# Kernel tuning notes

Hardware: AMD Instinct MI355X
Metric: run time of the kernel (lower is better)

Reference implementation:

```python
import jax, jax.numpy as jnp
import numpy as np

K = 7
TOWERS = 4
X_SIZE = 8
POS_SIZE = 3
NUM_GRAPHS = 128
NODES_PER_GRAPH = 512
N = NUM_GRAPHS * NODES_PER_GRAPH
EPS_STD = 1e-5  # PyG StdAggregation eps
BN_EPS = 1e-5
# degree histogram passed to PNAConv.__init__ -> avg log-degree used by scalers
_DEG_HIST = np.array([0, 0, 0, 0, 0, 100, 200, 700], dtype=np.float64)
_BINS = np.arange(_DEG_HIST.shape[0], dtype=np.float64)
AVG_DEG_LOG = float((np.log(_BINS + 1.0) * _DEG_HIST).sum() / _DEG_HIST.sum())


def knn_graph(pos, num_graphs, k):
    # batched kNN (loop=False): each node gets its k nearest neighbors within its graph
    Nn, D = pos.shape
    n = Nn // num_graphs
    p = pos.reshape(num_graphs, n, D)
    d2 = jnp.sum((p[:, :, None, :] - p[:, None, :, :]) ** 2, axis=-1)  # [B,n,n]
    d2 = d2 + jnp.eye(n, dtype=d2.dtype) * 1e10  # exclude self-loops
    _, idx = jax.lax.top_k(-d2, k)  # [B,n,k] local neighbor ids
    offs = (jnp.arange(num_graphs) * n)[:, None, None]
    return (idx + offs).reshape(Nn, k)  # global source ids per target node


def pna_conv(x, nbr, W_pre, b_pre, W_post, b_post, W_lin, b_lin):
    # PyG PNAConv, towers=4, pre_layers=1, post_layers=1, divide_input=False, edge_dim=None
    Nn, F = x.shape
    k = nbr.shape[1]
    x_j = x[nbr]                                              # gather sources [N,k,F]
    x_i = jnp.broadcast_to(x[:, None, :], (Nn, k, F))         # target features
    h = jnp.concatenate([x_i, x_j], axis=-1)                  # [N,k,2F]
    m = jnp.einsum('nke,tef->nktf', h, W_pre) + b_pre         # per-tower pre-MLP [N,k,T,F]
    mean = m.mean(axis=1)
    mn = m.min(axis=1)
    mx = m.max(axis=1)
    var = jnp.mean(m * m, axis=1) - mean * mean               # PyG VarAggregation
    std = jnp.sqrt(jax.nn.relu(var) + EPS_STD)
    agg = jnp.concatenate([mean, mn, mx, std], axis=-1)       # [N,T,4F]
    amp = jnp.log(k + 1.0) / AVG_DEG_LOG                      # deg == k for every node in a knn graph
    scaled = jnp.concatenate([agg, agg * amp, agg * (1.0 / amp)], axis=-1)  # identity/amp/atten [N,T,12F]
    out = jnp.concatenate([jnp.broadcast_to(x[:, None, :], (Nn, TOWERS, F)), scaled], axis=-1)  # [N,T,13F]
    out = jnp.einsum('ntg,tgf->ntf', out, W_post) + b_post    # per-tower post-MLP [N,T,F_out]
    out = out.reshape(Nn, -1)
    return out @ W_lin + b_lin                                # mixing Linear(out,out)


def batch_norm(x, g, b):
    # training-mode BatchNorm1d over the node dimension
    mu = x.mean(axis=0)
    var = x.var(axis=0)
    return g * (x - mu) * jax.lax.rsqrt(var + BN_EPS) + b


def forward(x, pos, W_pre1, b_pre1, W_post1, b_post1, W_lin1, b_lin1, bn1_g, bn1_b,
            W_pre2, b_pre2, W_post2, b_post2, W_lin2, b_lin2, bn2_g, bn2_b, num_graphs):
    nbr = knn_graph(pos, num_graphs, K)
    h = jax.nn.relu(batch_norm(pna_conv(x, nbr, W_pre1, b_pre1, W_post1, b_post1, W_lin1, b_lin1), bn1_g, bn1_b))
    h = jax.nn.relu(batch_norm(pna_conv(h, nbr, W_pre2, b_pre2, W_post2, b_post2, W_lin2, b_lin2), bn2_g, bn2_b))
    return h.reshape(num_graphs, -1, h.shape[-1]).mean(axis=1)  # global mean pool -> [B,128]


def _winit(key, shape):
    fan_in = shape[-2]
    return (jax.random.normal(key, shape, dtype=jnp.float32) / jnp.sqrt(jnp.float32(fan_in))).astype(jnp.float32)


def setup_inputs() -> dict:
    key = jax.random.key(0)
    ks = jax.random.split(key, 8)
    F1, F2 = X_SIZE, 64
    return {
        'x': jax.random.normal(ks[0], (N, X_SIZE), dtype=jnp.float32),
        'pos': jax.random.normal(ks[1], (N, POS_SIZE), dtype=jnp.float32),
        'W_pre1': _winit(ks[2], (TOWERS, 2 * F1, F1)),
        'b_pre1': jnp.zeros((TOWERS, F1), jnp.float32),
        'W_post1': _winit(ks[3], (TOWERS, 13 * F1, 64 // TOWERS)),
        'b_post1': jnp.zeros((TOWERS, 64 // TOWERS), jnp.float32),
        'W_lin1': _winit(ks[4], (64, 64)),
        'b_lin1': jnp.zeros((64,), jnp.float32),
        'bn1_g': jnp.ones((64,), jnp.float32),
        'bn1_b': jnp.zeros((64,), jnp.float32),
        'W_pre2': _winit(ks[5], (TOWERS, 2 * F2, F2)),
        'b_pre2': jnp.zeros((TOWERS, F2), jnp.float32),
        'W_post2': _winit(ks[6], (TOWERS, 13 * F2, 128 // TOWERS)),
        'b_post2': jnp.zeros((TOWERS, 128 // TOWERS), jnp.float32),
        'W_lin2': _winit(ks[7], (128, 128)),
        'b_lin2': jnp.zeros((128,), jnp.float32),
        'bn2_g': jnp.ones((128,), jnp.float32),
        'bn2_b': jnp.zeros((128,), jnp.float32),
        'num_graphs': NUM_GRAPHS,
    }


def reference(x, pos, W_pre1, b_pre1, W_post1, b_post1, W_lin1, b_lin1, bn1_g, bn1_b,
              W_pre2, b_pre2, W_post2, b_post2, W_lin2, b_lin2, bn2_g, bn2_b, num_graphs):
    return forward(x, pos, W_pre1, b_pre1, W_post1, b_post1, W_lin1, b_lin1, bn1_g, bn1_b,
                   W_pre2, b_pre2, W_post2, b_post2, W_lin2, b_lin2, bn2_g, bn2_b, num_graphs)
```

## Files before the change

kernel.cpp:

```cpp
#include <hip/hip_runtime.h>
#include <math.h>


#define NGRAPH 128
#define NPG    512
#define NN     (NGRAPH*NPG)
#define KNB    7

constexpr double AVG_DEG_LOG_D = 2.0239670479173344;
constexpr double LOG8_D        = 2.0794415416798357;

typedef _Float16 f16x8 __attribute__((ext_vector_type(8)));
typedef _Float16 h2    __attribute__((ext_vector_type(2)));
typedef float    f32x4 __attribute__((ext_vector_type(4)));

__device__ __forceinline__ unsigned short f2h(float x) {
    _Float16 h = (_Float16)x;
    return __builtin_bit_cast(unsigned short, h);
}

__global__ __launch_bounds__(256) void prep_kernel(
    const float* __restrict__ Wpost1, const float* __restrict__ Wpost2,
    const float* __restrict__ Wpre2,  const float* __restrict__ Wlin2,
    const float* __restrict__ Wlin1,  const float* __restrict__ bpost1,
    const float* __restrict__ blin1,
    const float* __restrict__ bpost2, const float* __restrict__ blin2,
    unsigned short* __restrict__ Wf1p, unsigned short* __restrict__ Wf1l,
    float* __restrict__ blin1_eff,
    unsigned short* __restrict__ Wfuv,
    unsigned short* __restrict__ Wfp, unsigned short* __restrict__ Wfl,
    float* __restrict__ blin_eff)
{
    const float AMP = (float)(LOG8_D / AVG_DEG_LOG_D);
    const float ATT = (float)(AVG_DEG_LOG_D / LOG8_D);
    for (int i = blockIdx.x*256 + threadIdx.x; i < 98496; i += gridDim.x*256) {
        if (i < 4096) {
            int t = i >> 10, kk = (i >> 9) & 1, lane = (i >> 3) & 63, j = i & 7;
            int k = kk*32 + ((lane >> 4) << 3) + j;
            int col = lane & 15;
            float val;
            if (k < 8)       val = Wpost1[(t*104 + k)*16 + col];
            else if (k < 40) {
                int g2 = k - 8;
                val = Wpost1[(t*104 +  8 + g2)*16 + col]
                    + AMP*Wpost1[(t*104 + 40 + g2)*16 + col]
                    + ATT*Wpost1[(t*104 + 72 + g2)*16 + col];
            } else val = 0.f;
            Wf1p[i] = f2h(val);
        } else if (i < 8192) {
            int jj = i - 4096;
            int kk = jj >> 11, tile = (jj >> 9) & 3, lane = (jj >> 3) & 63, j = jj & 7;
            int k = kk*32 + ((lane >> 4) << 3) + j;
            int col = tile*16 + (lane & 15);
            Wf1l[jj] = f2h(Wlin1[k*64 + col]);
        } else if (i < 8256) {
            int c = i - 8192;
            float s = blin1[c];
            for (int o = 0; o < 64; ++o) s += bpost1[o]*Wlin1[o*64 + c];
            blin1_eff[c] = s;
        } else if (i < 41024) {
            int jj = i - 8256;
            int kk = jj >> 14, ct = (jj >> 9) & 31, lane = (jj >> 3) & 63, jf = jj & 7;
            int k   = kk*32 + ((lane >> 4) << 3) + jf;
            int col = ct*16 + (lane & 15);
            float val;
            if (col < 256) { int t = col >> 6, f = col & 63; val = Wpre2[(t*128 +      k)*64 + f]; }
            else { int c2 = col - 256; int t = c2 >> 6, f = c2 & 63; val = Wpre2[(t*128 + 64 + k)*64 + f]; }
            Wfuv[jj] = f2h(val);
        } else if (i < 81984) {
            int jj = i - 41024;
            int t = jj / 10240, r = jj % 10240;
            int kk = r / 1024, r2 = r % 1024;
            int c = r2 >> 9, lane = (r2 >> 3) & 63, jf = r2 & 7;
            int G   = kk*32 + ((lane >> 4) << 3) + jf;
            int col = c*16 + (lane & 15);
            float val;
            if (G < 64) val = Wpost2[(t*832 + G)*32 + col];
            else {
                int g2 = G - 64;
                val = Wpost2[(t*832 +  64 + g2)*32 + col]
                    + AMP*Wpost2[(t*832 + 320 + g2)*32 + col]
                    + ATT*Wpost2[(t*832 + 576 + g2)*32 + col];
            }
            Wfp[jj] = f2h(val);
        } else if (i < 98368) {
            int jj = i - 81984;
            int kk = jj / 4096, r = jj % 4096;
            int tile = r >> 9, lane = (r >> 3) & 63, jf = r & 7;
            int k   = kk*32 + ((lane >> 4) << 3) + jf;
            int col = tile*16 + (lane & 15);
            Wfl[jj] = f2h(Wlin2[k*128 + col]);
        } else {
            int c = i - 98368;
            float s = blin2[c];
            for (int o = 0; o < 128; ++o) s += bpost2[o]*Wlin2[o*128 + c];
            blin_eff[c] = s;
        }
    }
}

__global__ __launch_bounds__(256) void knn_part_kernel(const float* __restrict__ pos, float2* __restrict__ part)
{
    __shared__ float4 cposS[128];
    const int b = blockIdx.x;
    const int g = b >> 3, h = (b >> 2) & 1, q = b & 3;
    const int gb = g * NPG;
    const int cbase = q * 128;
    if (threadIdx.x < 128) {
        int j = cbase + threadIdx.x;
        cposS[threadIdx.x] = make_float4(pos[(gb+j)*3+0], pos[(gb+j)*3+1], pos[(gb+j)*3+2], 0.f);
    }
    __syncthreads();
    const int i = h*256 + threadIdx.x;
    const float px = pos[(gb+i)*3+0], py = pos[(gb+i)*3+1], pz = pos[(gb+i)*3+2];
    float bd[KNB]; int bi[KNB];
#pragma unroll
    for (int e = 0; e < KNB; ++e) { bd[e] = 3.0e38f; bi[e] = -1; }
#pragma unroll 4
    for (int j = 0; j < 128; ++j) {
        float4 pj = cposS[j];
        float dx = px - pj.x, dy = py - pj.y, dz = pz - pj.z;
        float d2 = __fadd_rn(__fadd_rn(__fmul_rn(dx,dx), __fmul_rn(dy,dy)), __fmul_rn(dz,dz));
        if (cbase + j == i) d2 = __builtin_inff();
        bool cmp[KNB];
#pragma unroll
        for (int e = 0; e < KNB; ++e) cmp[e] = d2 < bd[e];
#pragma unroll
        for (int e = KNB-1; e >= 1; --e) {
            bd[e] = cmp[e-1] ? bd[e-1] : (cmp[e] ? d2 : bd[e]);
            bi[e] = cmp[e-1] ? bi[e-1] : (cmp[e] ? cbase + j : bi[e]);
        }
        bd[0] = cmp[0] ? d2 : bd[0];
        bi[0] = cmp[0] ? cbase + j : bi[0];
    }
    float2* dst = &part[((size_t)(g*NPG + i)*4 + q)*KNB];
#pragma unroll
    for (int e = 0; e < KNB; ++e) dst[e] = make_float2(bd[e], __int_as_float(bi[e]));
}

__global__ __launch_bounds__(256) void knn_merge_kernel(const float2* __restrict__ part, int* __restrict__ nbr)
{
    const int n = blockIdx.x*256 + threadIdx.x;
    const float4* p4 = (const float4*)&part[(size_t)n*28];
    float bd[KNB]; int bi[KNB];
#pragma unroll
    for (int e = 0; e < KNB; ++e) { bd[e] = 3.0e38f; bi[e] = -1; }
#pragma unroll
    for (int m4 = 0; m4 < 14; ++m4) {
        float4 pr = p4[m4];
#pragma unroll
        for (int half = 0; half < 2; ++half) {
            float d2  = half ? pr.z : pr.x;
            int   idx = __float_as_int(half ? pr.w : pr.y);
            bool cmp[KNB];
#pragma unroll
            for (int e = 0; e < KNB; ++e) cmp[e] = d2 < bd[e];
#pragma unroll
            for (int e = KNB-1; e >= 1; --e) {
                bd[e] = cmp[e-1] ? bd[e-1] : (cmp[e] ? d2 : bd[e]);
                bi[e] = cmp[e-1] ? bi[e-1] : (cmp[e] ? idx : bi[e]);
            }
            bd[0] = cmp[0] ? d2 : bd[0];
            bi[0] = cmp[0] ? idx : bi[0];
        }
    }
    const int gb = n & ~(NPG-1);
#pragma unroll
    for (int e = 0; e < KNB; ++e) nbr[n*KNB + e] = gb + bi[e];
}

__global__ __launch_bounds__(256) void a1_kernel(
    const float* __restrict__ x, const float* __restrict__ Wpre1, const float* __restrict__ bpre1,
    float* __restrict__ u1, float* __restrict__ v1)
{
    __shared__ float wS[512];
    __shared__ float bS[32];
    const int tid = threadIdx.x;
    wS[tid] = Wpre1[tid]; wS[tid+256] = Wpre1[tid+256];
    if (tid < 32) bS[tid] = bpre1[tid];
    __syncthreads();
    const int n  = blockIdx.x*8 + (tid>>5);
    const int tf = tid & 31;
    const int t = tf >> 3, f = tf & 7;
    float u = bS[tf], v = 0.f;
#pragma unroll
    for (int e = 0; e < 8; ++e) {
        float xv = x[n*8+e];
        u += xv * wS[(t*16 + e)*8 + f];
        v += xv * wS[(t*16 + 8 + e)*8 + f];
    }
    u1[n*32+tf] = u;
    v1[n*32+tf] = v;
}

__global__ __launch_bounds__(256) void b1_kernel(
    const float* __restrict__ x, const int* __restrict__ nbr,
    const float* __restrict__ u1, const float* __restrict__ v1,
    const unsigned short* __restrict__ Wf1p, const unsigned short* __restrict__ Wf1l,
    const float* __restrict__ blin1_eff,
    float* __restrict__ y1)
{
    __shared__ int nbrsS[112];
    __shared__ __align__(16) unsigned short actS[64*72];
    __shared__ __align__(16) unsigned short postS[16*72];
    const int tid  = threadIdx.x;
    const int base = blockIdx.x * 16;
    if (tid < 112) nbrsS[tid] = nbr[base*7 + tid];
    for (int i = tid; i < 384; i += 256) {
        int r = i / 6, gq = i - 6*r;
        *(ushort4*)&actS[r*72 + 40 + gq*4] = make_ushort4(0,0,0,0);
    }
#pragma unroll
    for (int it = 0; it < 2; ++it) {
        int i = tid + it*256;
        int n = i >> 5, r2 = i & 31, t = r2 >> 3, f = r2 & 7;
        actS[(n*4 + t)*72 + f] = f2h(x[(base+n)*8 + f]);
    }
    __syncthreads();
    {
        const int n = tid >> 4, cp = tid & 15;
        const int tf0 = cp*2, t = tf0 >> 3, f0 = tf0 & 7;
        float2 uu = *(const float2*)&u1[(base+n)*32 + tf0];
        float s0=0.f,s1=0.f,q0=0.f,q1=0.f;
        float mn0=3e38f,mn1=3e38f,mx0=-3e38f,mx1=-3e38f;
#pragma unroll
        for (int e = 0; e < 7; ++e) {
            float2 vv = *(const float2*)&v1[nbrsS[n*7+e]*32 + tf0];
            s0 += vv.x; q0 += vv.x*vv.x; mn0 = fminf(mn0, vv.x); mx0 = fmaxf(mx0, vv.x);
            s1 += vv.y; q1 += vv.y*vv.y; mn1 = fminf(mn1, vv.y); mx1 = fmaxf(mx1, vv.y);
        }
        float me0 = s0*(1.f/7.f), me1 = s1*(1.f/7.f);
        float sd0 = sqrtf(fmaxf(q0*(1.f/7.f) - me0*me0, 0.f) + 1e-5f);
        float sd1 = sqrtf(fmaxf(q1*(1.f/7.f) - me1*me1, 0.f) + 1e-5f);
        const int row = (n*4 + t)*72;
        ushort2 w_;
        w_.x = f2h(uu.x + me0); w_.y = f2h(uu.y + me1); *(ushort2*)&actS[row +  8 + f0] = w_;
        w_.x = f2h(uu.x + mn0); w_.y = f2h(uu.y + mn1); *(ushort2*)&actS[row + 16 + f0] = w_;
        w_.x = f2h(uu.x + mx0); w_.y = f2h(uu.y + mx1); *(ushort2*)&actS[row + 24 + f0] = w_;
        w_.x = f2h(sd0);        w_.y = f2h(sd1);        *(ushort2*)&actS[row + 32 + f0] = w_;
    }
    __syncthreads();
    const int l = tid & 63, w = tid >> 6;
    const int lr = l & 15, lk = l >> 4;
    f32x4 acc = {0.f,0.f,0.f,0.f};
    {
        const f16x8* WB = (const f16x8*)Wf1p;
#pragma unroll
        for (int kk = 0; kk < 2; ++kk) {
            f16x8 a = *(const f16x8*)&actS[(lr*4 + w)*72 + kk*32 + lk*8];
            f16x8 b = WB[(w*2 + kk)*64 + l];
            acc = __builtin_amdgcn_mfma_f32_16x16x32_f16(a, b, acc, 0, 0, 0);
        }
    }
#pragma unroll
    for (int j = 0; j < 4; ++j)
        postS[(lk*4 + j)*72 + w*16 + lr] = f2h(acc[j]);
    __syncthreads();
    f32x4 d = {0.f,0.f,0.f,0.f};
    {
        const f16x8* WB = (const f16x8*)Wf1l;
#pragma unroll
        for (int kk = 0; kk < 2; ++kk) {
            f16x8 a = *(const f16x8*)&postS[lr*72 + kk*32 + lk*8];
            f16x8 b = WB[(kk*4 + w)*64 + l];
            d = __builtin_amdgcn_mfma_f32_16x16x32_f16(a, b, d, 0, 0, 0);
        }
    }
    const float be = blin1_eff[w*16 + lr];
#pragma unroll
    for (int j = 0; j < 4; ++j)
        y1[(base + lk*4 + j)*64 + w*16 + lr] = d[j] + be;
}

template<int C>
__global__ __launch_bounds__(256) void bn_stats_kernel(
    const float* __restrict__ y, float* __restrict__ Ps, float* __restrict__ Pq)
{
    constexpr int IT     = (NN/1024)*(C/4)/256;
    constexpr int GROUPS = C/4;
    constexpr int REPS   = 256/GROUPS;
    const int tid = threadIdx.x;
    const float4* y4 = (const float4*)y + (size_t)blockIdx.x*256*IT;
    float4 s = make_float4(0.f,0.f,0.f,0.f), q = make_float4(0.f,0.f,0.f,0.f);
#pragma unroll
    for (int it = 0; it < IT; ++it) {
        float4 v = y4[it*256 + tid];
        s.x += v.x; s.y += v.y; s.z += v.z; s.w += v.w;
        q.x += v.x*v.x; q.y += v.y*v.y; q.z += v.z*v.z; q.w += v.w*v.w;
    }
    __shared__ float4 sS[256], qS[256];
    sS[tid] = s; qS[tid] = q;
    __syncthreads();
#pragma unroll
    for (int step = REPS/2; step >= 1; step >>= 1) {
        if (tid < step*GROUPS) {
            float4 s2 = sS[tid + step*GROUPS], q2 = qS[tid + step*GROUPS];
            float4 ss = sS[tid], qq = qS[tid];
            ss.x += s2.x; ss.y += s2.y; ss.z += s2.z; ss.w += s2.w;
            qq.x += q2.x; qq.y += q2.y; qq.z += q2.z; qq.w += q2.w;
            sS[tid] = ss; qS[tid] = qq;
        }
        __syncthreads();
    }
    if (tid < GROUPS) {
        ((float4*)&Ps[(size_t)blockIdx.x*C])[tid] = sS[tid];
        ((float4*)&Pq[(size_t)blockIdx.x*C])[tid] = qS[tid];
    }
}

template<int C>
__global__ __launch_bounds__(C) void finA_kernel(
    const float* __restrict__ Ps, const float* __restrict__ Pq,
    float* __restrict__ As, float* __restrict__ Aq)
{
    const int c = threadIdx.x, b = blockIdx.x;
    float s = 0.f, q = 0.f;
#pragma unroll
    for (int i = 0; i < 16; ++i) {
        s += Ps[(b*16 + i)*C + c];
        q += Pq[(b*16 + i)*C + c];
    }
    As[b*C + c] = s;
    Aq[b*C + c] = q;
}

template<int C>
__global__ __launch_bounds__(C) void fin_kernel(
    const float* __restrict__ As, const float* __restrict__ Aq,
    const float* __restrict__ g, const float* __restrict__ b,
    float* __restrict__ scO, float* __restrict__ shO)
{
    const int c = threadIdx.x;
    float s = 0.f, q = 0.f;
#pragma unroll 8
    for (int i = 0; i < 64; ++i) { s += As[i*C + c]; q += Aq[i*C + c]; }
    const float inv = 1.f/(float)NN;
    float mu  = s*inv;
    float var = q*inv - mu*mu;
    float sc  = g[c]*rsqrtf(var + 1e-5f);
    scO[c] = sc;
    shO[c] = b[c] - mu*sc;
}

__global__ __launch_bounds__(256) void a2_kernel(
    const float* __restrict__ y1raw, const float* __restrict__ sc1, const float* __restrict__ sh1,
    const unsigned short* __restrict__ Wfuv, const float* __restrict__ bpre2,
    unsigned short* __restrict__ uv2)
{
    __shared__ __align__(16) unsigned short a1S[64*72];
    __shared__ float biasS[256];
    const int tid  = threadIdx.x;
    const int base = blockIdx.x * 64;
    biasS[tid] = bpre2[tid];
#pragma unroll
    for (int it = 0; it < 4; ++it) {
        int i = tid + it*256;
        float4 vv = ((const float4*)y1raw)[blockIdx.x*1024 + i];
        int n = i >> 4, c0 = (i & 15)*4;
        float c_[4] = {vv.x, vv.y, vv.z, vv.w};
#pragma unroll
        for (int j = 0; j < 4; ++j) {
            int c = c0 + j;
            a1S[n*72 + c] = f2h(fmaxf(c_[j]*sc1[c] + sh1[c], 0.f));
        }
    }
    __syncthreads();
    const int l = tid & 63, w = tid >> 6;
    const int lr = l & 15, lk = l >> 4;
    const f16x8 a0  = *(const f16x8*)&a1S[(w*16 + lr)*72 +      lk*8];
    const f16x8 a1f = *(const f16x8*)&a1S[(w*16 + lr)*72 + 32 + lk*8];
    const f16x8* WB = (const f16x8*)Wfuv;
#pragma unroll 4
    for (int ct = 0; ct < 32; ++ct) {
        f32x4 acc = {0.f,0.f,0.f,0.f};
        f16x8 b0 = WB[ct*64 + l];
        f16x8 b1 = WB[(32 + ct)*64 + l];
        acc = __builtin_amdgcn_mfma_f32_16x16x32_f16(a0,  b0, acc, 0, 0, 0);
        acc = __builtin_amdgcn_mfma_f32_16x16x32_f16(a1f, b1, acc, 0, 0, 0);
        const int col = ct*16 + lr;
        const float bias = (ct < 16) ? biasS[col] : 0.f;
#pragma unroll
        for (int j = 0; j < 4; ++j)
            uv2[(base + w*16 + lk*4 + j)*512 + col] = f2h(acc[j] + bias);
    }
}

__global__ __launch_bounds__(256) void b2_kernel(
    const int* __restrict__ nbr, const float* __restrict__ y1raw,
    const float* __restrict__ sc1, const float* __restrict__ sh1,
    const unsigned short* __restrict__ uv2,
    const unsigned short* __restrict__ Wfp, const unsigned short* __restrict__ Wfl,
    const float* __restrict__ blin_eff,
    float* __restrict__ y2)
{
    __shared__ int nbrsS[112];
    __shared__ __align__(16) unsigned short a1S[16*72];
    __shared__ __align__(16) unsigned short aggS[64*264];
    __shared__ __align__(16) unsigned short postS[16*136];

    const int tid = threadIdx.x;
    const int ob   = blockIdx.x;
    const int xcd  = ob & 7, slot = ob >> 3;
    const int gph  = ((slot >> 5) << 3) + xcd;
    const int sub  = slot & 31;
    const int base = gph*NPG + sub*16;

    if (tid < 112) nbrsS[tid] = nbr[base*7 + tid];
    for (int i = tid; i < 1024; i += 256) {
        int c = i & 63, n = i >> 6;
        float a = fmaxf(y1raw[base*64 + i]*sc1[c] + sh1[c], 0.f);
        a1S[n*72 + c] = f2h(a);
    }
    __syncthreads();
    {
        const int ns = tid >> 6, cg = tid & 63;
        const int t = cg >> 4, f0 = (cg & 15) * 4;
        const h2 inv7 = { (_Float16)(1.f/7.f), (_Float16)(1.f/7.f) };
#pragma unroll
        for (int it = 0; it < 4; ++it) {
            const int ln = it*4 + ns;
            uint2 uu = *(const uint2*)&uv2[(size_t)(base+ln)*512 + cg*4];
            h2 u01 = __builtin_bit_cast(h2, uu.x);
            h2 u23 = __builtin_bit_cast(h2, uu.y);
            h2 z = { (_Float16)0.f, (_Float16)0.f };
            h2 s01 = z, s23 = z, q01 = z, q23 = z;
            h2 mn01 = { (_Float16)65504.f, (_Float16)65504.f }, mn23 = mn01;
            h2 mx01 = { (_Float16)-65504.f, (_Float16)-65504.f }, mx23 = mx01;
#pragma unroll
            for (int e = 0; e < 7; ++e) {
                uint2 vv = *(const uint2*)&uv2[(size_t)nbrsS[ln*7+e]*512 + 256 + cg*4];
                h2 v01 = __builtin_bit_cast(h2, vv.x);
                h2 v23 = __builtin_bit_cast(h2, vv.y);
                s01 += v01; s23 += v23;
                q01 += v01*v01; q23 += v23*v23;
                mn01 = __builtin_elementwise_min(mn01, v01);
                mn23 = __builtin_elementwise_min(mn23, v23);
                mx01 = __builtin_elementwise_max(mx01, v01);
                mx23 = __builtin_elementwise_max(mx23, v23);
            }
            h2 me01 = s01*inv7, me23 = s23*inv7;
            h2 om01 = u01 + me01, om23 = u23 + me23;
            h2 on01 = u01 + mn01, on23 = u23 + mn23;
            h2 ox01 = u01 + mx01, ox23 = u23 + mx23;
            float m0 = (float)me01[0], m1 = (float)me01[1];
            float m2 = (float)me23[0], m3 = (float)me23[1];
            float sd0 = sqrtf(fmaxf(fmaf((float)q01[0], 1.f/7.f, -m0*m0), 0.f) + 1e-5f);
            float sd1 = sqrtf(fmaxf(fmaf((float)q01[1], 1.f/7.f, -m1*m1), 0.f) + 1e-5f);
            float sd2 = sqrtf(fmaxf(fmaf((float)q23[0], 1.f/7.f, -m2*m2), 0.f) + 1e-5f);
            float sd3 = sqrtf(fmaxf(fmaf((float)q23[1], 1.f/7.f, -m3*m3), 0.f) + 1e-5f);
            h2 sd01 = { (_Float16)sd0, (_Float16)sd1 };
            h2 sd23 = { (_Float16)sd2, (_Float16)sd3 };
            const int ro = (t*16 + ln)*264 + f0;
            *(uint2*)&aggS[ro      ] = make_uint2(__builtin_bit_cast(unsigned, om01), __builtin_bit_cast(unsigned, om23));
            *(uint2*)&aggS[ro +  64] = make_uint2(__builtin_bit_cast(unsigned, on01), __builtin_bit_cast(unsigned, on23));
            *(uint2*)&aggS[ro + 128] = make_uint2(__builtin_bit_cast(unsigned, ox01), __builtin_bit_cast(unsigned, ox23));
            *(uint2*)&aggS[ro + 192] = make_uint2(__builtin_bit_cast(unsigned, sd01), __builtin_bit_cast(unsigned, sd23));
        }
    }
    __syncthreads();
    const int l = tid & 63, w = tid >> 6;
    const int lr = l & 15, lk = l >> 4;
    f32x4 acc0 = {0.f,0.f,0.f,0.f}, acc1 = {0.f,0.f,0.f,0.f};
    {
        const f16x8* WB = (const f16x8*)Wfp;
#pragma unroll
        for (int kk = 0; kk < 10; ++kk) {
            f16x8 a;
            if (kk < 2) a = *(const f16x8*)&a1S[lr*72 + kk*32 + lk*8];
            else        a = *(const f16x8*)&aggS[(w*16 + lr)*264 + (kk-2)*32 + lk*8];
            f16x8 b0 = WB[((w*10 + kk)*2 + 0)*64 + l];
            f16x8 b1 = WB[((w*10 + kk)*2 + 1)*64 + l];
            acc0 = __builtin_amdgcn_mfma_f32_16x16x32_f16(a, b0, acc0, 0, 0, 0);
            acc1 = __builtin_amdgcn_mfma_f32_16x16x32_f16(a, b1, acc1, 0, 0, 0);
        }
    }
#pragma unroll
    for (int j = 0; j < 4; ++j) {
        const int row = lk*4 + j;
        postS[row*136 + w*32 +      lr] = f2h(acc0[j]);
        postS[row*136 + w*32 + 16 + lr] = f2h(acc1[j]);
    }
    __syncthreads();
    f32x4 d0 = {0.f,0.f,0.f,0.f}, d1 = {0.f,0.f,0.f,0.f};
    {
        const f16x8* WB = (const f16x8*)Wfl;
#pragma unroll
        for (int kk = 0; kk < 4; ++kk) {
            f16x8 a = *(const f16x8*)&postS[lr*136 + kk*32 + lk*8];
            f16x8 b0 = WB[(kk*8 + 2*w + 0)*64 + l];
            f16x8 b1 = WB[(kk*8 + 2*w + 1)*64 + l];
            d0 = __builtin_amdgcn_mfma_f32_16x16x32_f16(a, b0, d0, 0, 0, 0);
            d1 = __builtin_amdgcn_mfma_f32_16x16x32_f16(a, b1, d1, 0, 0, 0);
        }
    }
    const float be0 = blin_eff[w*32 +      lr];
    const float be1 = blin_eff[w*32 + 16 + lr];
#pragma unroll
    for (int j = 0; j < 4; ++j) {
        const int row = lk*4 + j;
        y2[(base + row)*128 + w*32 +      lr] = d0[j] + be0;
        y2[(base + row)*128 + w*32 + 16 + lr] = d1[j] + be1;
    }
}

__global__ __launch_bounds__(128) void pool_part_kernel(
    const float* __restrict__ y2, const float* __restrict__ sc2, const float* __restrict__ sh2,
    float* __restrict__ Pp)
{
    const int c = threadIdx.x;
    const int b = blockIdx.x;
    const float sc = sc2[c];
    const float sh = sh2[c];
    float acc = 0.f;
    const size_t base = (size_t)b*64*128 + c;
#pragma unroll 4
    for (int i = 0; i < 64; ++i)
        acc += fmaxf(y2[base + (size_t)i*128]*sc + sh, 0.f);
    Pp[b*128 + c] = acc;
}

__global__ __launch_bounds__(128) void pool_fin_kernel(
    const float* __restrict__ Pp, float* __restrict__ out)
{
    const int c = threadIdx.x, g = blockIdx.x;
    float acc = 0.f;
#pragma unroll
    for (int i = 0; i < 8; ++i) acc += Pp[(g*8 + i)*128 + c];
    out[g*128 + c] = acc * (1.f/(float)NPG);
}

extern "C" void kernel_launch(void* const* d_in, const int* in_sizes, int n_in,
                              void* d_out, int out_size, void* d_ws, size_t ws_size,
                              hipStream_t stream)
{
    const float* x      = (const float*)d_in[0];
    const float* pos    = (const float*)d_in[1];
    const float* Wpre1  = (const float*)d_in[2];
    const float* bpre1  = (const float*)d_in[3];
    const float* Wpost1 = (const float*)d_in[4];
    const float* bpost1 = (const float*)d_in[5];
    const float* Wlin1  = (const float*)d_in[6];
    const float* blin1  = (const float*)d_in[7];
    const float* bn1g   = (const float*)d_in[8];
    const float* bn1b   = (const float*)d_in[9];
    const float* Wpre2  = (const float*)d_in[10];
    const float* bpre2  = (const float*)d_in[11];
    const float* Wpost2 = (const float*)d_in[12];
    const float* bpost2 = (const float*)d_in[13];
    const float* Wlin2  = (const float*)d_in[14];
    const float* blin2  = (const float*)d_in[15];
    const float* bn2g   = (const float*)d_in[16];
    const float* bn2b   = (const float*)d_in[17];
    float* out = (float*)d_out;

    char* ws = (char*)d_ws;
    size_t off = 0;
    auto alloc = [&](size_t bytes) { void* p = ws + off; off += (bytes + 255) & ~(size_t)255; return p; };
    int*    nbr  = (int*)   alloc((size_t)NN*7*4);
    float2* part = (float2*)alloc((size_t)NN*28*8);
    float* u1    = (float*)alloc((size_t)NN*32*4);
    float* v1    = (float*)alloc((size_t)NN*32*4);
    float* y1    = (float*)alloc((size_t)NN*64*4);
    unsigned short* uv2 = (unsigned short*)alloc((size_t)NN*512*2);
    float* y2    = (float*)alloc((size_t)NN*128*4);
    unsigned short* Wf1p = (unsigned short*)alloc(4096*2);
    unsigned short* Wf1l = (unsigned short*)alloc(4096*2);
    float* blin1_eff = (float*)alloc(64*4);
    unsigned short* Wfuv = (unsigned short*)alloc(32768*2);
    unsigned short* Wfp  = (unsigned short*)alloc(40960*2);
    unsigned short* Wfl  = (unsigned short*)alloc(16384*2);
    float* blin_eff = (float*)alloc(128*4);
    float* P1s   = (float*)alloc(1024*64*4);
    float* P1q   = (float*)alloc(1024*64*4);
    float* A1s   = (float*)alloc(64*64*4);
    float* A1q   = (float*)alloc(64*64*4);
    float* sc1   = (float*)alloc(64*4);
    float* sh1   = (float*)alloc(64*4);
    float* P2s   = (float*)alloc(1024*128*4);
    float* P2q   = (float*)alloc(1024*128*4);
    float* A2s   = (float*)alloc(64*128*4);
    float* A2q   = (float*)alloc(64*128*4);
    float* sc2   = (float*)alloc(128*4);
    float* sh2   = (float*)alloc(128*4);
    float* Pp    = (float*)alloc(1024*128*4);

    prep_kernel<<<128, 256, 0, stream>>>(Wpost1, Wpost2, Wpre2, Wlin2, Wlin1, bpost1, blin1,
                                         bpost2, blin2,
                                         Wf1p, Wf1l, blin1_eff, Wfuv, Wfp, Wfl, blin_eff);
    knn_part_kernel<<<NGRAPH*8, 256, 0, stream>>>(pos, part);
    knn_merge_kernel<<<NN/256, 256, 0, stream>>>(part, nbr);
    a1_kernel<<<NN/8, 256, 0, stream>>>(x, Wpre1, bpre1, u1, v1);
    b1_kernel<<<NN/16, 256, 0, stream>>>(x, nbr, u1, v1, Wf1p, Wf1l, blin1_eff, y1);
    bn_stats_kernel<64><<<1024, 256, 0, stream>>>(y1, P1s, P1q);
    finA_kernel<64><<<64, 64, 0, stream>>>(P1s, P1q, A1s, A1q);
    fin_kernel<64><<<1, 64, 0, stream>>>(A1s, A1q, bn1g, bn1b, sc1, sh1);
    a2_kernel<<<NN/64, 256, 0, stream>>>(y1, sc1, sh1, Wfuv, bpre2, uv2);
    b2_kernel<<<NN/16, 256, 0, stream>>>(nbr, y1, sc1, sh1, uv2, Wfp, Wfl, blin_eff, y2);
    bn_stats_kernel<128><<<1024, 256, 0, stream>>>(y2, P2s, P2q);
    finA_kernel<128><<<64, 128, 0, stream>>>(P2s, P2q, A2s, A2q);
    fin_kernel<128><<<1, 128, 0, stream>>>(A2s, A2q, bn2g, bn2b, sc2, sh2);
    pool_part_kernel<<<1024, 128, 0, stream>>>(y2, sc2, sh2, Pp);
    pool_fin_kernel<<<NGRAPH, 128, 0, stream>>>(Pp, out);
}
```

Before: 175.7 us.

## Fold layer-2 target-side pre-MLP term into post-MLP weights and bias

The target-side contribution u = x_i·W_pre_top + b_pre is identical across neighbors, so it adds as a constant shift to the mean, min and max aggregates. It is therefore folded algebraically into a precomputed weight matrix Wfu (W_pre_top times the summed post weights) and into the effective bias. a2 now computes and stores only the neighbor-side v (256 columns instead of 512), which halves the uv2 write and read traffic. b2 adds two extra MFMA k-steps on the node features and drops the per-element u additions. A small extra prep kernel computes the folded bias, and the change relies on std being unaffected by the shift.

```diff
diff --git a/kernel.cpp b/kernel.cpp
--- a/kernel.cpp
+++ b/kernel.cpp
@@ -24,16 +24,14 @@
     const float* __restrict__ Wpre2,  const float* __restrict__ Wlin2,
     const float* __restrict__ Wlin1,  const float* __restrict__ bpost1,
     const float* __restrict__ blin1,
-    const float* __restrict__ bpost2, const float* __restrict__ blin2,
     unsigned short* __restrict__ Wf1p, unsigned short* __restrict__ Wf1l,
     float* __restrict__ blin1_eff,
-    unsigned short* __restrict__ Wfuv,
-    unsigned short* __restrict__ Wfp, unsigned short* __restrict__ Wfl,
-    float* __restrict__ blin_eff)
+    unsigned short* __restrict__ Wfv, unsigned short* __restrict__ Wfu,
+    unsigned short* __restrict__ Wfp, unsigned short* __restrict__ Wfl)
 {
     const float AMP = (float)(LOG8_D / AVG_DEG_LOG_D);
     const float ATT = (float)(AVG_DEG_LOG_D / LOG8_D);
-    for (int i = blockIdx.x*256 + threadIdx.x; i < 98496; i += gridDim.x*256) {
+    for (int i = blockIdx.x*256 + threadIdx.x; i < 90176; i += gridDim.x*256) {
         if (i < 4096) {
             int t = i >> 10, kk = (i >> 9) & 1, lane = (i >> 3) & 63, j = i & 7;
             int k = kk*32 + ((lane >> 4) << 3) + j;
@@ -58,17 +56,33 @@
             float s = blin1[c];
             for (int o = 0; o < 64; ++o) s += bpost1[o]*Wlin1[o*64 + c];
             blin1_eff[c] = s;
-        } else if (i < 41024) {
+        } else if (i < 24640) {
             int jj = i - 8256;
-            int kk = jj >> 14, ct = (jj >> 9) & 31, lane = (jj >> 3) & 63, jf = jj & 7;
+            int kk = jj >> 13, ct = (jj >> 9) & 15, lane = (jj >> 3) & 63, jf = jj & 7;
             int k   = kk*32 + ((lane >> 4) << 3) + jf;
             int col = ct*16 + (lane & 15);
-            float val;
-            if (col < 256) { int t = col >> 6, f = col & 63; val = Wpre2[(t*128 +      k)*64 + f]; }
-            else { int c2 = col - 256; int t = c2 >> 6, f = c2 & 63; val = Wpre2[(t*128 + 64 + k)*64 + f]; }
-            Wfuv[jj] = f2h(val);
-        } else if (i < 81984) {
-            int jj = i - 41024;
+            int t = col >> 6, f = col & 63;
+            Wfv[jj] = f2h(Wpre2[(t*128 + 64 + k)*64 + f]);
+        } else if (i < 32832) {
+            int jj = i - 24640;
+            int t = jj >> 11, kk = (jj >> 10) & 1, c = (jj >> 9) & 1, lane = (jj >> 3) & 63, jf = jj & 7;
+            int k   = kk*32 + ((lane >> 4) << 3) + jf;
+            int col = c*16 + (lane & 15);
+            float acc = 0.f;
+            for (int f = 0; f < 64; ++f) {
+                float wu = 0.f;
+#pragma unroll
+                for (int s = 0; s < 3; ++s) {
+                    int g2 = s*64 + f;
+                    wu += Wpost2[(t*832 +  64 + g2)*32 + col]
+                        + AMP*Wpost2[(t*832 + 320 + g2)*32 + col]
+                        + ATT*Wpost2[(t*832 + 576 + g2)*32 + col];
+                }
+                acc += Wpre2[(t*128 + k)*64 + f] * wu;
+            }
+            Wfu[jj] = f2h(acc);
+        } else if (i < 73792) {
+            int jj = i - 32832;
             int t = jj / 10240, r = jj % 10240;
             int kk = r / 1024, r2 = r % 1024;
             int c = r2 >> 9, lane = (r2 >> 3) & 63, jf = r2 & 7;
@@ -83,20 +97,44 @@
                     + ATT*Wpost2[(t*832 + 576 + g2)*32 + col];
             }
             Wfp[jj] = f2h(val);
-        } else if (i < 98368) {
-            int jj = i - 81984;
+        } else {
+            int jj = i - 73792;
             int kk = jj / 4096, r = jj % 4096;
             int tile = r >> 9, lane = (r >> 3) & 63, jf = r & 7;
             int k   = kk*32 + ((lane >> 4) << 3) + jf;
             int col = tile*16 + (lane & 15);
             Wfl[jj] = f2h(Wlin2[k*128 + col]);
-        } else {
-            int c = i - 98368;
-            float s = blin2[c];
-            for (int o = 0; o < 128; ++o) s += bpost2[o]*Wlin2[o*128 + c];
-            blin_eff[c] = s;
-        }
-    }
+        }
+    }
+}
+
+__global__ __launch_bounds__(128) void prep2_kernel(
+    const float* __restrict__ Wpost2, const float* __restrict__ bpre2,
+    const float* __restrict__ bpost2, const float* __restrict__ blin2,
+    const float* __restrict__ Wlin2,  float* __restrict__ blin_eff)
+{
+    const float AMP = (float)(LOG8_D / AVG_DEG_LOG_D);
+    const float ATT = (float)(AVG_DEG_LOG_D / LOG8_D);
+    __shared__ float buS[128];
+    const int o = threadIdx.x;
+    const int t = o >> 5, col = o & 31;
+    float bu = 0.f;
+    for (int f = 0; f < 64; ++f) {
+        float wu = 0.f;
+#pragma unroll
+        for (int s = 0; s < 3; ++s) {
+            int g2 = s*64 + f;
+            wu += Wpost2[(t*832 +  64 + g2)*32 + col]
+                + AMP*Wpost2[(t*832 + 320 + g2)*32 + col]
+                + ATT*Wpost2[(t*832 + 576 + g2)*32 + col];
+        }
+        bu += bpre2[t*64 + f] * wu;
+    }
+    buS[o] = bu + bpost2[o];
+    __syncthreads();
+    float s = blin2[o];
+    for (int k = 0; k < 128; ++k) s += buS[k]*Wlin2[k*128 + o];
+    blin_eff[o] = s;
 }
 
 __global__ __launch_bounds__(256) void knn_part_kernel(const float* __restrict__ pos, float2* __restrict__ part)
@@ -344,14 +382,12 @@
 
 __global__ __launch_bounds__(256) void a2_kernel(
     const float* __restrict__ y1raw, const float* __restrict__ sc1, const float* __restrict__ sh1,
-    const unsigned short* __restrict__ Wfuv, const float* __restrict__ bpre2,
-    unsigned short* __restrict__ uv2)
+    const unsigned short* __restrict__ Wfv,
+    unsigned short* __restrict__ v2)
 {
     __shared__ __align__(16) unsigned short a1S[64*72];
-    __shared__ float biasS[256];
     const int tid  = threadIdx.x;
     const int base = blockIdx.x * 64;
-    biasS[tid] = bpre2[tid];
 #pragma unroll
     for (int it = 0; it < 4; ++it) {
         int i = tid + it*256;
@@ -369,26 +405,26 @@
     const int lr = l & 15, lk = l >> 4;
     const f16x8 a0  = *(const f16x8*)&a1S[(w*16 + lr)*72 +      lk*8];
     const f16x8 a1f = *(const f16x8*)&a1S[(w*16 + lr)*72 + 32 + lk*8];
-    const f16x8* WB = (const f16x8*)Wfuv;
+    const f16x8* WB = (const f16x8*)Wfv;
 #pragma unroll 4
-    for (int ct = 0; ct < 32; ++ct) {
+    for (int ct = 0; ct < 16; ++ct) {
         f32x4 acc = {0.f,0.f,0.f,0.f};
         f16x8 b0 = WB[ct*64 + l];
-        f16x8 b1 = WB[(32 + ct)*64 + l];
+        f16x8 b1 = WB[(16 + ct)*64 + l];
         acc = __builtin_amdgcn_mfma_f32_16x16x32_f16(a0,  b0, acc, 0, 0, 0);
         acc = __builtin_amdgcn_mfma_f32_16x16x32_f16(a1f, b1, acc, 0, 0, 0);
         const int col = ct*16 + lr;
-        const float bias = (ct < 16) ? biasS[col] : 0.f;
 #pragma unroll
         for (int j = 0; j < 4; ++j)
-            uv2[(base + w*16 + lk*4 + j)*512 + col] = f2h(acc[j] + bias);
+            v2[(size_t)(base + w*16 + lk*4 + j)*256 + col] = f2h(acc[j]);
     }
 }
 
 __global__ __launch_bounds__(256) void b2_kernel(
     const int* __restrict__ nbr, const float* __restrict__ y1raw,
     const float* __restrict__ sc1, const float* __restrict__ sh1,
-    const unsigned short* __restrict__ uv2,
+    const unsigned short* __restrict__ v2,
+    const unsigned short* __restrict__ Wfu,
     const unsigned short* __restrict__ Wfp, const unsigned short* __restrict__ Wfl,
     const float* __restrict__ blin_eff,
     float* __restrict__ y2)
@@ -419,16 +455,13 @@
 #pragma unroll
         for (int it = 0; it < 4; ++it) {
             const int ln = it*4 + ns;
-            uint2 uu = *(const uint2*)&uv2[(size_t)(base+ln)*512 + cg*4];
-            h2 u01 = __builtin_bit_cast(h2, uu.x);
-            h2 u23 = __builtin_bit_cast(h2, uu.y);
             h2 z = { (_Float16)0.f, (_Float16)0.f };
             h2 s01 = z, s23 = z, q01 = z, q23 = z;
             h2 mn01 = { (_Float16)65504.f, (_Float16)65504.f }, mn23 = mn01;
             h2 mx01 = { (_Float16)-65504.f, (_Float16)-65504.f }, mx23 = mx01;
 #pragma unroll
             for (int e = 0; e < 7; ++e) {
-                uint2 vv = *(const uint2*)&uv2[(size_t)nbrsS[ln*7+e]*512 + 256 + cg*4];
+                uint2 vv = *(const uint2*)&v2[(size_t)nbrsS[ln*7+e]*256 + cg*4];
                 h2 v01 = __builtin_bit_cast(h2, vv.x);
                 h2 v23 = __builtin_bit_cast(h2, vv.y);
                 s01 += v01; s23 += v23;
@@ -439,9 +472,6 @@
                 mx23 = __builtin_elementwise_max(mx23, v23);
             }
             h2 me01 = s01*inv7, me23 = s23*inv7;
-            h2 om01 = u01 + me01, om23 = u23 + me23;
-            h2 on01 = u01 + mn01, on23 = u23 + mn23;
-            h2 ox01 = u01 + mx01, ox23 = u23 + mx23;
             float m0 = (float)me01[0], m1 = (float)me01[1];
             float m2 = (float)me23[0], m3 = (float)me23[1];
             float sd0 = sqrtf(fmaxf(fmaf((float)q01[0], 1.f/7.f, -m0*m0), 0.f) + 1e-5f);
@@ -451,9 +481,9 @@
             h2 sd01 = { (_Float16)sd0, (_Float16)sd1 };
             h2 sd23 = { (_Float16)sd2, (_Float16)sd3 };
             const int ro = (t*16 + ln)*264 + f0;
-            *(uint2*)&aggS[ro      ] = make_uint2(__builtin_bit_cast(unsigned, om01), __builtin_bit_cast(unsigned, om23));
-            *(uint2*)&aggS[ro +  64] = make_uint2(__builtin_bit_cast(unsigned, on01), __builtin_bit_cast(unsigned, on23));
-            *(uint2*)&aggS[ro + 128] = make_uint2(__builtin_bit_cast(unsigned, ox01), __builtin_bit_cast(unsigned, ox23));
+            *(uint2*)&aggS[ro      ] = make_uint2(__builtin_bit_cast(unsigned, me01), __builtin_bit_cast(unsigned, me23));
+            *(uint2*)&aggS[ro +  64] = make_uint2(__builtin_bit_cast(unsigned, mn01), __builtin_bit_cast(unsigned, mn23));
+            *(uint2*)&aggS[ro + 128] = make_uint2(__builtin_bit_cast(unsigned, mx01), __builtin_bit_cast(unsigned, mx23));
             *(uint2*)&aggS[ro + 192] = make_uint2(__builtin_bit_cast(unsigned, sd01), __builtin_bit_cast(unsigned, sd23));
         }
     }
@@ -462,14 +492,24 @@
     const int lr = l & 15, lk = l >> 4;
     f32x4 acc0 = {0.f,0.f,0.f,0.f}, acc1 = {0.f,0.f,0.f,0.f};
     {
-        const f16x8* WB = (const f16x8*)Wfp;
-#pragma unroll
-        for (int kk = 0; kk < 10; ++kk) {
-            f16x8 a;
-            if (kk < 2) a = *(const f16x8*)&a1S[lr*72 + kk*32 + lk*8];
-            else        a = *(const f16x8*)&aggS[(w*16 + lr)*264 + (kk-2)*32 + lk*8];
-            f16x8 b0 = WB[((w*10 + kk)*2 + 0)*64 + l];
-            f16x8 b1 = WB[((w*10 + kk)*2 + 1)*64 + l];
+        const f16x8* WP = (const f16x8*)Wfp;
+        const f16x8* WU = (const f16x8*)Wfu;
+#pragma unroll
+        for (int kk = 0; kk < 12; ++kk) {
+            f16x8 a, b0, b1;
+            if (kk < 2) {
+                a  = *(const f16x8*)&a1S[lr*72 + kk*32 + lk*8];
+                b0 = WP[((w*10 + kk)*2 + 0)*64 + l];
+                b1 = WP[((w*10 + kk)*2 + 1)*64 + l];
+            } else if (kk < 4) {
+                a  = *(const f16x8*)&a1S[lr*72 + (kk-2)*32 + lk*8];
+                b0 = WU[((w*2 + (kk-2))*2 + 0)*64 + l];
+                b1 = WU[((w*2 + (kk-2))*2 + 1)*64 + l];
+            } else {
+                a  = *(const f16x8*)&aggS[(w*16 + lr)*264 + (kk-4)*32 + lk*8];
+                b0 = WP[((w*10 + (kk-2))*2 + 0)*64 + l];
+                b1 = WP[((w*10 + (kk-2))*2 + 1)*64 + l];
+            }
             acc0 = __builtin_amdgcn_mfma_f32_16x16x32_f16(a, b0, acc0, 0, 0, 0);
             acc1 = __builtin_amdgcn_mfma_f32_16x16x32_f16(a, b1, acc1, 0, 0, 0);
         }
@@ -561,14 +601,15 @@
     float* u1    = (float*)alloc((size_t)NN*32*4);
     float* v1    = (float*)alloc((size_t)NN*32*4);
     float* y1    = (float*)alloc((size_t)NN*64*4);
-    unsigned short* uv2 = (unsigned short*)alloc((size_t)NN*512*2);
+    unsigned short* v2 = (unsigned short*)alloc((size_t)NN*256*2);
     float* y2    = (float*)alloc((size_t)NN*128*4);
     unsigned short* Wf1p = (unsigned short*)alloc(4096*2);
     unsigned short* Wf1l = (unsigned short*)alloc(4096*2);
     float* blin1_eff = (float*)alloc(64*4);
-    unsigned short* Wfuv = (unsigned short*)alloc(32768*2);
-    unsigned short* Wfp  = (unsigned short*)alloc(40960*2);
-    unsigned short* Wfl  = (unsigned short*)alloc(16384*2);
+    unsigned short* Wfv = (unsigned short*)alloc(16384*2);
+    unsigned short* Wfu = (unsigned short*)alloc(8192*2);
+    unsigned short* Wfp = (unsigned short*)alloc(40960*2);
+    unsigned short* Wfl = (unsigned short*)alloc(16384*2);
     float* blin_eff = (float*)alloc(128*4);
     float* P1s   = (float*)alloc(1024*64*4);
     float* P1q   = (float*)alloc(1024*64*4);
@@ -585,8 +626,8 @@
     float* Pp    = (float*)alloc(1024*128*4);
 
     prep_kernel<<<128, 256, 0, stream>>>(Wpost1, Wpost2, Wpre2, Wlin2, Wlin1, bpost1, blin1,
-                                         bpost2, blin2,
-                                         Wf1p, Wf1l, blin1_eff, Wfuv, Wfp, Wfl, blin_eff);
+                                         Wf1p, Wf1l, blin1_eff, Wfv, Wfu, Wfp, Wfl);
+    prep2_kernel<<<1, 128, 0, stream>>>(Wpost2, bpre2, bpost2, blin2, Wlin2, blin_eff);
     knn_part_kernel<<<NGRAPH*8, 256, 0, stream>>>(pos, part);
     knn_merge_kernel<<<NN/256, 256, 0, stream>>>(part, nbr);
     a1_kernel<<<NN/8, 256, 0, stream>>>(x, Wpre1, bpre1, u1, v1);
@@ -594,8 +635,8 @@
     bn_stats_kernel<64><<<1024, 256, 0, stream>>>(y1, P1s, P1q);
     finA_kernel<64><<<64, 64, 0, stream>>>(P1s, P1q, A1s, A1q);
     fin_kernel<64><<<1, 64, 0, stream>>>(A1s, A1q, bn1g, bn1b, sc1, sh1);
-    a2_kernel<<<NN/64, 256, 0, stream>>>(y1, sc1, sh1, Wfuv, bpre2, uv2);
-    b2_kernel<<<NN/16, 256, 0, stream>>>(nbr, y1, sc1, sh1, uv2, Wfp, Wfl, blin_eff, y2);
+    a2_kernel<<<NN/64, 256, 0, stream>>>(y1, sc1, sh1, Wfv, v2);
+    b2_kernel<<<NN/16, 256, 0, stream>>>(nbr, y1, sc1, sh1, v2, Wfu, Wfp, Wfl, blin_eff, y2);
     bn_stats_kernel<128><<<1024, 256, 0, stream>>>(y2, P2s, P2q);
     finA_kernel<128><<<64, 128, 0, stream>>>(P2s, P2q, A2s, A2q);
     fin_kernel<128><<<1, 128, 0, stream>>>(A2s, A2q, bn2g, bn2b, sc2, sh2);
```

Result: slower. 192.6 us (+9.6%).
